# Kernel optimization log

Measured on AMD Instinct MI355X. Metric: run time of the kernel, lower is better.

Reference implementation:

```python
import jax, jax.numpy as jnp
import numpy as np

L, H, E, FF, MAXP, NKNOW = 4, 8, 512, 2048, 10, 1000
B, S = 4, 128
HD = E // H


def _layer_norm(x, g, b, eps=1e-5):
    m = x.mean(-1, keepdims=True)
    v = ((x - m) ** 2).mean(-1, keepdims=True)
    return (x - m) / jnp.sqrt(v + eps) * g + b


def setup_inputs() -> dict:
    key = jax.random.key(0)
    ks = jax.random.split(key, 16)
    x = jax.random.normal(ks[0], (B, S, E), jnp.float32)
    adj = jax.random.randint(ks[1], (B, S, S), 0, 2, jnp.int32)
    s_mask = jax.random.randint(ks[2], (B, S, S), 0, 2, jnp.int32)
    o_mask = jax.random.randint(ks[3], (B, S, S), 0, 2, jnp.int32)
    knowledge = jax.random.normal(ks[4], (NKNOW, E), jnp.float32)
    know_adj = jax.random.randint(ks[5], (B, S, S), 0, NKNOW, jnp.int64)
    pos_mask = jax.random.randint(ks[6], (S, S), 0, MAXP + 1, jnp.int32)
    # relative position embedding tables (padding_idx=0 -> row 0 zero)
    pe_k = jax.random.normal(ks[7], (MAXP + 1, HD), jnp.float32).at[0].set(0.0)
    pe_v = jax.random.normal(ks[8], (MAXP + 1, HD), jnp.float32).at[0].set(0.0)
    sc = 0.02
    # stacked per-layer parameters
    Wq = jax.random.normal(ks[9], (L, E, E), jnp.float32) * sc
    Wk = jax.random.normal(ks[10], (L, E, E), jnp.float32) * sc
    Wvs = jax.random.normal(ks[11], (L, E, E), jnp.float32) * sc
    Wvo = jax.random.normal(ks[12], (L, E, E), jnp.float32) * sc
    Wo = jax.random.normal(ks[13], (L, E, E), jnp.float32) * sc
    Wkn = jax.random.normal(ks[14], (L, E, E), jnp.float32) * sc
    kf = jax.random.split(ks[15], 4)
    w1 = jax.random.normal(kf[0], (L, FF, E), jnp.float32) * sc
    b1 = jnp.zeros((L, FF), jnp.float32)
    w2 = jax.random.normal(kf[1], (L, E, FF), jnp.float32) * sc
    b2 = jnp.zeros((L, E), jnp.float32)
    ln1_g = jnp.ones((L, E), jnp.float32)
    ln1_b = jnp.zeros((L, E), jnp.float32)
    ln2_g = jnp.ones((L, E), jnp.float32)
    ln2_b = jnp.zeros((L, E), jnp.float32)
    return dict(x=x, adj=adj, s_mask=s_mask, o_mask=o_mask, knowledge=knowledge,
                know_adj=know_adj, pos_mask=pos_mask, pe_k=pe_k, pe_v=pe_v,
                Wq=Wq, Wk=Wk, Wvs=Wvs, Wvo=Wvo, Wo=Wo, Wkn=Wkn,
                ln1_g=ln1_g, ln1_b=ln1_b, w1=w1, b1=b1, w2=w2, b2=b2,
                ln2_g=ln2_g, ln2_b=ln2_b)


def reference(x, adj, s_mask, o_mask, knowledge, know_adj, pos_mask, pe_k, pe_v,
              Wq, Wk, Wvs, Wvo, Wo, Wkn, ln1_g, ln1_b, w1, b1, w2, b2,
              ln2_g, ln2_b):
    bsz, slen, emb = x.shape
    hd = emb // H
    scaling = float(hd) ** (-0.5)
    # relative position embeddings, shared across batch/heads: [S,S,hd]
    pos = jnp.clip(pos_mask, 0, MAXP)
    rel_k = pe_k[pos]
    rel_v = pe_v[pos]
    adj_f = adj.astype(x.dtype)[:, None, :, :]          # [B,1,S,S]
    sm = s_mask.astype(x.dtype)[:, None, :, :, None]    # [B,1,S,S,1]
    om = o_mask.astype(x.dtype)[:, None, :, :, None]
    know_feat = knowledge[know_adj]                      # [B,S,S,E]

    def split_heads(t):  # [B,S,E] -> [B,H,S,hd]
        return t.reshape(bsz, slen, H, hd).transpose(0, 2, 1, 3)

    h = x
    for i in range(L):
        q = split_heads(h @ Wq[i].T)
        k = split_heads(h @ Wk[i].T)
        vs = split_heads(h @ Wvs[i].T)
        vo = split_heads(h @ Wvo[i].T)
        # knowledge projection -> [B,H,S,S,hd]
        know = (know_feat @ Wkn[i].T).reshape(bsz, slen, slen, H, hd).transpose(0, 3, 1, 2, 4)
        # multiplicative attention: q_i * (k_j + know_ij + rel_ij) summed over hd
        rel = (know + rel_k[None, None]) + k[:, :, None, :, :]
        scores = jnp.einsum('bhid,bhijd->bhij', q, rel) * scaling
        scores = scores - (1.0 - adj_f) * 1e30          # mask_logic
        attn = jax.nn.softmax(scores, axis=-1)           # [B,H,S,S]
        value = vs[:, :, None, :, :] * sm + vo[:, :, None, :, :] * om  # [B,H,S,S,hd]
        attn_sum = jnp.einsum('bhijd,bhij->bhid', value + rel_v[None, None], attn)
        out = attn_sum.transpose(0, 2, 1, 3).reshape(bsz, slen, emb) @ Wo[i].T
        h = _layer_norm(h + out, ln1_g[i], ln1_b[i])
        ff = jax.nn.relu(h @ w1[i].T + b1[i]) @ w2[i].T + b2[i]
        h = _layer_norm(h + ff, ln2_g[i], ln2_b[i])
    return h
```

## Files before the change

### kernel.cpp

```cpp
#include <hip/hip_runtime.h>

#define EE 512
#define SS 128
#define BB 4
#define NH 8
#define HD 64
#define FFD 2048
#define NL 4
#define LDQ 2048

typedef short bf16x8 __attribute__((ext_vector_type(8)));
typedef float f32x4 __attribute__((ext_vector_type(4)));

__device__ __forceinline__ ushort f2bf(float f) {
    uint u = __float_as_uint(f);
    return (ushort)((u + 0x7fffu + ((u >> 16) & 1u)) >> 16);
}
__device__ __forceinline__ float bflo(uint u) { return __uint_as_float(u << 16); }
__device__ __forceinline__ float bfhi(uint u) { return __uint_as_float(u & 0xffff0000u); }

__device__ __forceinline__ void gll16(const ushort* g, ushort* l) {
    __builtin_amdgcn_global_load_lds(
        (const __attribute__((address_space(1))) void*)g,
        (__attribute__((address_space(3))) void*)l, 16, 0, 0);
}

struct GemmJob {
    const ushort* A; const ushort* B;
    float* Cf; ushort* Cb;
    const float* bias; const float* resid;
    int M, N, K, flags, nbx, base;
};

__global__ __launch_bounds__(256) void gemm_bf16(GemmJob j0, GemmJob j1, int njobs)
{
    __shared__ ushort As[3][2048];
    __shared__ ushort Bs[3][4096];
    GemmJob j = (njobs > 1 && (int)blockIdx.x >= j1.base) ? j1 : j0;
    const int bid = (int)blockIdx.x - j.base;
    const int by = bid / j.nbx, bx = bid % j.nbx;
    const int rowBase = by * 32, colBase = bx * 64;
    const int t = threadIdx.x, lane = t & 63, wid = t >> 6;
    const int wc = wid;
    const int Kd = j.K, Md = j.M, Nd = j.N;

    const ushort* Bg = j.B + (size_t)(colBase + lane) * Kd;
    int gr = rowBase + (lane & 31); if (gr >= Md) gr = Md - 1;
    const ushort* Ag = j.A + (size_t)gr * Kd + (2 * wid + (lane >> 5)) * 8;

    f32x4 acc[2];
#pragma unroll
    for (int m = 0; m < 2; ++m)
#pragma unroll
        for (int r = 0; r < 4; ++r) acc[m][r] = 0.f;

    auto STAGE = [&](int bf, int tt) {
        const int k0 = tt << 6;
        gll16(Bg + k0 + (2 * wid) * 8,     &Bs[bf][(2 * wid) * 512]);
        gll16(Bg + k0 + (2 * wid + 1) * 8, &Bs[bf][(2 * wid + 1) * 512]);
        gll16(Ag + k0,                     &As[bf][(2 * wid) * 256]);
    };
    auto COMPUTE = [&](int bf) {
#pragma unroll
        for (int kc = 0; kc < 2; ++kc) {
            const int c16 = kc * 4 + (lane >> 4);
            bf16x8 af[2], bfg;
#pragma unroll
            for (int m = 0; m < 2; ++m) {
                const int row = m * 16 + (lane & 15);
                af[m] = *(const bf16x8*)&As[bf][c16 * 256 + row * 8];
            }
            {
                const int rowb = wc * 16 + (lane & 15);
                bfg = *(const bf16x8*)&Bs[bf][c16 * 512 + rowb * 8];
            }
#pragma unroll
            for (int m = 0; m < 2; ++m)
                acc[m] = __builtin_amdgcn_mfma_f32_16x16x32_bf16(af[m], bfg, acc[m], 0, 0, 0);
        }
    };

    const int nt = Kd >> 6;
    STAGE(0, 0);
    STAGE(1, 1);
    asm volatile("s_waitcnt vmcnt(3)" ::: "memory");
    __builtin_amdgcn_s_barrier();
    int bc = 0, bs = 2;
    for (int tt = 0; tt < nt; ++tt) {
        const bool more = (tt + 2) < nt;
        if (more) STAGE(bs, tt + 2);
        COMPUTE(bc);
        if (tt < nt - 1) {
            if (more) asm volatile("s_waitcnt vmcnt(3)" ::: "memory");
            else      asm volatile("s_waitcnt vmcnt(0)" ::: "memory");
            __builtin_amdgcn_s_barrier();
        }
        bc = bc == 2 ? 0 : bc + 1;
        bs = bs == 2 ? 0 : bs + 1;
    }

    const int cl = lane & 15, rh = lane >> 4;
#pragma unroll
    for (int m = 0; m < 2; ++m) {
        const int col = colBase + wc * 16 + cl;
        const int row0 = rowBase + m * 16 + rh * 4;
#pragma unroll
        for (int r = 0; r < 4; ++r) {
            const int rr = row0 + r;
            if (rr < Md) {
                float v = acc[m][r];
                if (j.flags & 1) v += j.bias[col];
                if (j.flags & 2) v = fmaxf(v, 0.f);
                if (j.resid) v += j.resid[(size_t)rr * Nd + col];
                if (j.Cf) j.Cf[(size_t)rr * Nd + col] = v;
                if (j.Cb) j.Cb[(size_t)rr * Nd + col] = f2bf(v);
            }
        }
    }
}

struct PrepArgs {
    const float *Wq, *Wk, *Wvs, *Wvo, *Wo, *Wkn, *w1, *w2, *know, *x;
    ushort *wqkvv, *wo, *wkn, *w1b, *w2b, *knowb, *hb;
    float *h;
};
#define P4_WQKVV 1048576
#define P4_B1 (P4_WQKVV + 262144)
#define P4_B2 (P4_B1 + 262144)
#define P4_B3 (P4_B2 + 1048576)
#define P4_B4 (P4_B3 + 1048576)
#define P4_B5 (P4_B4 + 128000)
#define P4_TOT (P4_B5 + 65536)

__global__ __launch_bounds__(256) void prep_kernel(PrepArgs p)
{
    const int i = blockIdx.x * 256 + threadIdx.x;
    if (i >= P4_TOT) return;
    const float4* src;
    ushort4* dst;
    if (i < P4_WQKVV) {
        const int l = i >> 18, r = i & 262143, q = r >> 16;
        const float* s = (q == 0 ? p.Wq : q == 1 ? p.Wk : q == 2 ? p.Wvs : p.Wvo);
        src = (const float4*)s + l * 65536 + (r & 65535);
        dst = (ushort4*)p.wqkvv + i;
    } else if (i < P4_B1) {
        const int k = i - P4_WQKVV;
        src = (const float4*)p.Wo + k; dst = (ushort4*)p.wo + k;
    } else if (i < P4_B2) {
        const int k = i - P4_B1;
        src = (const float4*)p.Wkn + k; dst = (ushort4*)p.wkn + k;
    } else if (i < P4_B3) {
        const int k = i - P4_B2;
        src = (const float4*)p.w1 + k; dst = (ushort4*)p.w1b + k;
    } else if (i < P4_B4) {
        const int k = i - P4_B3;
        src = (const float4*)p.w2 + k; dst = (ushort4*)p.w2b + k;
    } else if (i < P4_B5) {
        const int k = i - P4_B4;
        src = (const float4*)p.know + k; dst = (ushort4*)p.knowb + k;
    } else {
        const int k = i - P4_B5;
        src = (const float4*)p.x + k; dst = (ushort4*)p.hb + k;
        ((float4*)p.h)[k] = *src;
    }
    float4 v = *src;
    ushort4 o; o.x = f2bf(v.x); o.y = f2bf(v.y); o.z = f2bf(v.z); o.w = f2bf(v.w);
    *dst = o;
}

__global__ __launch_bounds__(256) void ln_kernel(
    const float* __restrict__ X, const float* __restrict__ g,
    const float* __restrict__ bt, float* __restrict__ Yf,
    ushort* __restrict__ Yb, int rows)
{
    const int w = threadIdx.x >> 6, lane = threadIdx.x & 63;
    const int row = blockIdx.x * 4 + w;
    if (row >= rows) return;
    const float* x = X + (size_t)row * EE;
    float4 v0 = ((const float4*)x)[lane];
    float4 v1 = ((const float4*)x)[lane + 64];
    float s  = v0.x + v0.y + v0.z + v0.w + v1.x + v1.y + v1.z + v1.w;
    float q2 = v0.x*v0.x + v0.y*v0.y + v0.z*v0.z + v0.w*v0.w
             + v1.x*v1.x + v1.y*v1.y + v1.z*v1.z + v1.w*v1.w;
#pragma unroll
    for (int o = 32; o; o >>= 1) { s += __shfl_xor(s, o); q2 += __shfl_xor(q2, o); }
    const float mean = s * (1.f / EE);
    const float var  = q2 * (1.f / EE) - mean * mean;
    const float rstd = rsqrtf(var + 1e-5f);
    float4 g0 = ((const float4*)g)[lane],  g1 = ((const float4*)g)[lane + 64];
    float4 b0 = ((const float4*)bt)[lane], b1 = ((const float4*)bt)[lane + 64];
    float4 o0, o1;
    o0.x = (v0.x - mean) * rstd * g0.x + b0.x;
    o0.y = (v0.y - mean) * rstd * g0.y + b0.y;
    o0.z = (v0.z - mean) * rstd * g0.z + b0.z;
    o0.w = (v0.w - mean) * rstd * g0.w + b0.w;
    o1.x = (v1.x - mean) * rstd * g1.x + b1.x;
    o1.y = (v1.y - mean) * rstd * g1.y + b1.y;
    o1.z = (v1.z - mean) * rstd * g1.z + b1.z;
    o1.w = (v1.w - mean) * rstd * g1.w + b1.w;
    float* y = Yf + (size_t)row * EE;
    ((float4*)y)[lane] = o0;
    ((float4*)y)[lane + 64] = o1;
    ushort* yb = Yb + (size_t)row * EE;
    ushort4 p0, p1;
    p0.x = f2bf(o0.x); p0.y = f2bf(o0.y); p0.z = f2bf(o0.z); p0.w = f2bf(o0.w);
    p1.x = f2bf(o1.x); p1.y = f2bf(o1.y); p1.z = f2bf(o1.z); p1.w = f2bf(o1.w);
    ((ushort4*)yb)[lane] = p0;
    ((ushort4*)yb)[lane + 64] = p1;
}

__global__ __launch_bounds__(256) void attn_kernel(
    const ushort* __restrict__ qkvv, const ushort* __restrict__ kproj,
    const int* __restrict__ know_adj, const int* __restrict__ pos_mask,
    const float* __restrict__ pe_k, const float* __restrict__ pe_v,
    const int* __restrict__ adj, const int* __restrict__ s_mask,
    const int* __restrict__ o_mask, ushort* __restrict__ asum)
{
    const int blk = blockIdx.x;
    const int b = blk >> 7, i = blk & 127;
    const int t = threadIdx.x;

    __shared__ float q_s[EE];
    __shared__ float sc[NH][SS];
    __shared__ float qpe[NH][11];
    __shared__ float ap[NH][11];
    __shared__ float ws_s[SS], wo_s[SS];
    __shared__ int   pos_s[SS], n_s[SS], adj_s[SS];

    if (t < 64) {
        uint4 v = *(const uint4*)(qkvv + (size_t)(b * SS + i) * LDQ + t * 8);
        float* qd = q_s + t * 8;
        qd[0] = bflo(v.x); qd[1] = bfhi(v.x); qd[2] = bflo(v.y); qd[3] = bfhi(v.y);
        qd[4] = bflo(v.z); qd[5] = bfhi(v.z); qd[6] = bflo(v.w); qd[7] = bfhi(v.w);
    } else if (t >= 128) {
        const int jj = t - 128;
        const size_t off = ((size_t)(b * SS + i)) * SS + jj;
        n_s[jj]   = know_adj[off];
        adj_s[jj] = adj[off];
        ws_s[jj]  = (float)s_mask[off];
        wo_s[jj]  = (float)o_mask[off];
        int p = pos_mask[i * SS + jj];
        pos_s[jj] = p > 10 ? 10 : (p < 0 ? 0 : p);
    }
    __syncthreads();

    if (t < NH * 11) {
        const int h = t / 11, p = t % 11;
        const float* pk = pe_k + p * HD;
        const float* qh = q_s + h * HD;
        float a = 0.f;
#pragma unroll
        for (int d = 0; d < HD; ++d) a += qh[d] * pk[d];
        qpe[h][p] = a;
        ap[h][p] = 0.f;
    }
    __syncthreads();

    {
        const int jj = t >> 1, s = t & 1;
        const uint4* kp4 = (const uint4*)(kproj + (size_t)n_s[jj] * LDQ + s * 256);
        const uint4* kr4 = (const uint4*)(qkvv + (size_t)(b * SS + jj) * LDQ + EE + s * 256);
        const float amask = adj_s[jj] ? 0.f : 1e30f;
        const int p = pos_s[jj];
#pragma unroll
        for (int h4 = 0; h4 < 4; ++h4) {
            const int h = s * 4 + h4;
            const float* qh = q_s + h * HD;
            float a = 0.f;
#pragma unroll
            for (int dv = 0; dv < 8; ++dv) {
                uint4 kv = kr4[h4 * 8 + dv];
                uint4 pv = kp4[h4 * 8 + dv];
                const float* q8 = qh + dv * 8;
                a += q8[0] * (bflo(kv.x) + bflo(pv.x));
                a += q8[1] * (bfhi(kv.x) + bfhi(pv.x));
                a += q8[2] * (bflo(kv.y) + bflo(pv.y));
                a += q8[3] * (bfhi(kv.y) + bfhi(pv.y));
                a += q8[4] * (bflo(kv.z) + bflo(pv.z));
                a += q8[5] * (bfhi(kv.z) + bfhi(pv.z));
                a += q8[6] * (bflo(kv.w) + bflo(pv.w));
                a += q8[7] * (bfhi(kv.w) + bfhi(pv.w));
            }
            sc[h][jj] = (a + qpe[h][p]) * 0.125f - amask;
        }
    }
    __syncthreads();

    {
        const int w = t >> 6, lane = t & 63;
#pragma unroll
        for (int hh = 0; hh < 2; ++hh) {
            const int h = w * 2 + hh;
            float v0 = sc[h][lane], v1 = sc[h][lane + 64];
            float m = fmaxf(v0, v1);
#pragma unroll
            for (int o = 32; o; o >>= 1) m = fmaxf(m, __shfl_xor(m, o));
            float e0 = __expf(v0 - m), e1 = __expf(v1 - m);
            float ssum = e0 + e1;
#pragma unroll
            for (int o = 32; o; o >>= 1) ssum += __shfl_xor(ssum, o);
            const float inv = 1.f / ssum;
            e0 *= inv; e1 *= inv;
            sc[h][lane] = e0; sc[h][lane + 64] = e1;
            atomicAdd(&ap[h][pos_s[lane]], e0);
            atomicAdd(&ap[h][pos_s[lane + 64]], e1);
        }
    }
    __syncthreads();

    {
        const int h = t >> 5, d0 = (t & 31) * 2;
        float a0 = 0.f, a1 = 0.f;
        const ushort* vbase = qkvv + (size_t)b * SS * LDQ + 1024 + h * HD + d0;
#pragma unroll 4
        for (int jj = 0; jj < SS; ++jj) {
            const float aw = sc[h][jj];
            const float wsj = ws_s[jj], woj = wo_s[jj];
            const ushort* r = vbase + (size_t)jj * LDQ;
            const uint vsp = *(const uint*)r;
            const uint vop = *(const uint*)(r + 512);
            a0 += aw * (wsj * bflo(vsp) + woj * bflo(vop));
            a1 += aw * (wsj * bfhi(vsp) + woj * bfhi(vop));
        }
#pragma unroll
        for (int p = 0; p < 11; ++p) {
            const float apv = ap[h][p];
            a0 += apv * pe_v[p * HD + d0];
            a1 += apv * pe_v[p * HD + d0 + 1];
        }
        const uint o = (uint)f2bf(a0) | ((uint)f2bf(a1) << 16);
        *(uint*)(asum + (size_t)(b * SS + i) * EE + h * HD + d0) = o;
    }
}

extern "C" void kernel_launch(void* const* d_in, const int* in_sizes, int n_in,
                              void* d_out, int out_size, void* d_ws, size_t ws_size,
                              hipStream_t stream)
{
    const float* x         = (const float*)d_in[0];
    const int*   adj       = (const int*)d_in[1];
    const int*   s_mask    = (const int*)d_in[2];
    const int*   o_mask    = (const int*)d_in[3];
    const float* knowledge = (const float*)d_in[4];
    const int*   know_adj  = (const int*)d_in[5];
    const int*   pos_mask  = (const int*)d_in[6];
    const float* pe_k      = (const float*)d_in[7];
    const float* pe_v      = (const float*)d_in[8];
    const float* Wq        = (const float*)d_in[9];
    const float* Wk        = (const float*)d_in[10];
    const float* Wvs       = (const float*)d_in[11];
    const float* Wvo       = (const float*)d_in[12];
    const float* Wo        = (const float*)d_in[13];
    const float* Wkn       = (const float*)d_in[14];
    const float* ln1_g     = (const float*)d_in[15];
    const float* ln1_b     = (const float*)d_in[16];
    const float* w1        = (const float*)d_in[17];
    const float* b1        = (const float*)d_in[18];
    const float* w2        = (const float*)d_in[19];
    const float* b2        = (const float*)d_in[20];
    const float* ln2_g     = (const float*)d_in[21];
    const float* ln2_b     = (const float*)d_in[22];

    const int NTOK = BB * SS;
    const size_t NTE = (size_t)NTOK * EE;

    float*  h      = (float*)d_ws;
    float*  xt     = h + NTE;
    ushort* hb     = (ushort*)(xt + NTE);
    ushort* qkvv   = hb + NTE;
    ushort* kprojb = qkvv + (size_t)NTOK * LDQ;
    ushort* asumb  = kprojb + (size_t)1024 * LDQ;
    ushort* ffnb   = asumb + NTE;
    ushort* wqkvv  = ffnb + (size_t)NTOK * FFD;
    ushort* wob    = wqkvv + (size_t)NL * 4 * EE * EE;
    ushort* wknb   = wob + (size_t)NL * EE * EE;
    ushort* w1b    = wknb + (size_t)NL * EE * EE;
    ushort* w2b    = w1b + (size_t)NL * FFD * EE;
    ushort* knowb  = w2b + (size_t)NL * EE * FFD;

    PrepArgs pa;
    pa.Wq = Wq; pa.Wk = Wk; pa.Wvs = Wvs; pa.Wvo = Wvo; pa.Wo = Wo; pa.Wkn = Wkn;
    pa.w1 = w1; pa.w2 = w2; pa.know = knowledge; pa.x = x;
    pa.wqkvv = wqkvv; pa.wo = wob; pa.wkn = wknb; pa.w1b = w1b; pa.w2b = w2b;
    pa.knowb = knowb; pa.hb = hb; pa.h = h;
    prep_kernel<<<dim3((P4_TOT + 255) / 256), dim3(256), 0, stream>>>(pa);

    const dim3 blk(256);
    for (int l = 0; l < NL; ++l) {
        GemmJob jq{};
        jq.A = hb; jq.B = wqkvv + (size_t)l * 4 * EE * EE;
        jq.Cb = qkvv; jq.M = NTOK; jq.N = 4 * EE; jq.K = EE;
        jq.nbx = 32; jq.base = 0;
        if (l == 0) {
            GemmJob jk{};
            jk.A = knowb; jk.B = wknb;
            jk.Cb = kprojb; jk.M = 1000; jk.N = NL * EE; jk.K = EE;
            jk.nbx = 32; jk.base = 512;
            gemm_bf16<<<dim3(512 + 1024), blk, 0, stream>>>(jq, jk, 2);
        } else {
            gemm_bf16<<<dim3(512), blk, 0, stream>>>(jq, jq, 1);
        }

        attn_kernel<<<dim3(NTOK), blk, 0, stream>>>(qkvv, kprojb + (size_t)l * EE,
                                                    know_adj, pos_mask,
                                                    pe_k, pe_v, adj, s_mask, o_mask, asumb);

        GemmJob jo{};
        jo.A = asumb; jo.B = wob + (size_t)l * EE * EE;
        jo.Cf = xt; jo.resid = h; jo.M = NTOK; jo.N = EE; jo.K = EE;
        jo.nbx = 8; jo.base = 0;
        gemm_bf16<<<dim3(128), blk, 0, stream>>>(jo, jo, 1);

        ln_kernel<<<dim3(128), blk, 0, stream>>>(xt, ln1_g + l * EE, ln1_b + l * EE,
                                                 h, hb, NTOK);

        GemmJob jf1{};
        jf1.A = hb; jf1.B = w1b + (size_t)l * FFD * EE;
        jf1.Cb = ffnb; jf1.bias = b1 + (size_t)l * FFD; jf1.flags = 3;
        jf1.M = NTOK; jf1.N = FFD; jf1.K = EE; jf1.nbx = 32; jf1.base = 0;
        gemm_bf16<<<dim3(512), blk, 0, stream>>>(jf1, jf1, 1);

        GemmJob jf2{};
        jf2.A = ffnb; jf2.B = w2b + (size_t)l * EE * FFD;
        jf2.Cf = xt; jf2.bias = b2 + (size_t)l * EE; jf2.resid = h; jf2.flags = 1;
        jf2.M = NTOK; jf2.N = EE; jf2.K = FFD; jf2.nbx = 8; jf2.base = 0;
        gemm_bf16<<<dim3(128), blk, 0, stream>>>(jf2, jf2, 1);

        float* lnout = (l == NL - 1) ? (float*)d_out : h;
        ln_kernel<<<dim3(128), blk, 0, stream>>>(xt, ln2_g + l * EE, ln2_b + l * EE,
                                                 lnout, hb, NTOK);
    }
}
```

Measured before the change: 578.2 us.

## Precompute attention score terms with MFMA GEMMs instead of per-pair dot products

Splits the score q·(k + know + rel_k) into three parts. The q·k part comes from a batched per-head MFMA GEMM. The q·know and q·pe_k parts come from one GEMM of every query against all 1000 knowledge projections plus 11 position-embedding rows, which are placed after the knowledge rows in the kproj buffer. The attention kernel then only gathers these precomputed scalars, which removes the per-(i,j) 64-wide gather dot products over bf16 rows. The value loop is also restructured to batch its loads. The trade-off is an extra kernel launch and large fp32 intermediates (qkk is 512×8192) written to and read back from global memory, which computes scores for all 1000 knowledge rows even though only gathered entries are used.

```diff
diff --git a/kernel.cpp b/kernel.cpp
--- a/kernel.cpp
+++ b/kernel.cpp
@@ -119,9 +119,79 @@
     }
 }
 
+__global__ __launch_bounds__(256) void score_gemm(
+    const ushort* __restrict__ qkvv, const ushort* __restrict__ kprojl,
+    float* __restrict__ qk, float* __restrict__ qkk)
+{
+    __shared__ ushort As[2048];
+    __shared__ ushort Bs[4096];
+    const int t = threadIdx.x, lane = t & 63, wid = t >> 6;
+    const int bid = blockIdx.x;
+    const ushort *Abase, *Bbase;
+    float* Cbase; int crs, rowBase, colBase;
+    if (bid < 256) {
+        const int q = bid >> 3, sub = bid & 7;
+        const int b = q >> 3, h = q & 7;
+        rowBase = (sub >> 1) * 32; colBase = (sub & 1) * 64;
+        Abase = qkvv + (size_t)(b * SS) * LDQ + h * HD;
+        Bbase = qkvv + (size_t)(b * SS) * LDQ + 512 + h * HD;
+        Cbase = qk + (size_t)b * 131072 + h * 128;
+        crs = 1024;
+    } else {
+        const int idx = bid - 256;
+        const int h = idx >> 8, sub = idx & 255;
+        rowBase = (sub >> 4) * 32; colBase = (sub & 15) * 64;
+        Abase = qkvv + h * HD;
+        Bbase = kprojl + h * HD;
+        Cbase = qkk + (size_t)h * 1024;
+        crs = 8192;
+    }
+    {
+        const ushort* Bg = Bbase + (size_t)(colBase + lane) * LDQ;
+        const ushort* Ag = Abase + (size_t)(rowBase + (lane & 31)) * LDQ
+                           + (2 * wid + (lane >> 5)) * 8;
+        gll16(Bg + (2 * wid) * 8,     &Bs[(2 * wid) * 512]);
+        gll16(Bg + (2 * wid + 1) * 8, &Bs[(2 * wid + 1) * 512]);
+        gll16(Ag,                     &As[(2 * wid) * 256]);
+        asm volatile("s_waitcnt vmcnt(0)" ::: "memory");
+        __builtin_amdgcn_s_barrier();
+    }
+    f32x4 acc[2];
+#pragma unroll
+    for (int m = 0; m < 2; ++m)
+#pragma unroll
+        for (int r = 0; r < 4; ++r) acc[m][r] = 0.f;
+#pragma unroll
+    for (int kc = 0; kc < 2; ++kc) {
+        const int c16 = kc * 4 + (lane >> 4);
+        bf16x8 af[2], bfg;
+#pragma unroll
+        for (int m = 0; m < 2; ++m) {
+            const int row = m * 16 + (lane & 15);
+            af[m] = *(const bf16x8*)&As[c16 * 256 + row * 8];
+        }
+        {
+            const int rowb = wid * 16 + (lane & 15);
+            bfg = *(const bf16x8*)&Bs[c16 * 512 + rowb * 8];
+        }
+#pragma unroll
+        for (int m = 0; m < 2; ++m)
+            acc[m] = __builtin_amdgcn_mfma_f32_16x16x32_bf16(af[m], bfg, acc[m], 0, 0, 0);
+    }
+    const int cl = lane & 15, rh = lane >> 4;
+#pragma unroll
+    for (int m = 0; m < 2; ++m) {
+        const int col = colBase + wid * 16 + cl;
+        const int row0 = rowBase + m * 16 + rh * 4;
+#pragma unroll
+        for (int r = 0; r < 4; ++r)
+            Cbase[(size_t)(row0 + r) * crs + col] = acc[m][r];
+    }
+}
+
 struct PrepArgs {
-    const float *Wq, *Wk, *Wvs, *Wvo, *Wo, *Wkn, *w1, *w2, *know, *x;
-    ushort *wqkvv, *wo, *wkn, *w1b, *w2b, *knowb, *hb;
+    const float *Wq, *Wk, *Wvs, *Wvo, *Wo, *Wkn, *w1, *w2, *know, *x, *pek;
+    ushort *wqkvv, *wo, *wkn, *w1b, *w2b, *knowb, *hb, *kpe;
     float *h;
 };
 #define P4_WQKVV 1048576
@@ -130,9 +200,10 @@
 #define P4_B3 (P4_B2 + 1048576)
 #define P4_B4 (P4_B3 + 1048576)
 #define P4_B5 (P4_B4 + 128000)
-#define P4_TOT (P4_B5 + 65536)
-
-__global__ __launch_bounds__(256) void prep_kernel(PrepArgs p)
+#define P4_B6 (P4_B5 + 65536)
+#define P4_TOT (P4_B6 + 5632)
+
+__global__ __launch_bounds__(256) void prep_kernel(PrepArgs pa)
 {
     const int i = blockIdx.x * 256 + threadIdx.x;
     if (i >= P4_TOT) return;
@@ -140,28 +211,34 @@
     ushort4* dst;
     if (i < P4_WQKVV) {
         const int l = i >> 18, r = i & 262143, q = r >> 16;
-        const float* s = (q == 0 ? p.Wq : q == 1 ? p.Wk : q == 2 ? p.Wvs : p.Wvo);
+        const float* s = (q == 0 ? pa.Wq : q == 1 ? pa.Wk : q == 2 ? pa.Wvs : pa.Wvo);
         src = (const float4*)s + l * 65536 + (r & 65535);
-        dst = (ushort4*)p.wqkvv + i;
+        dst = (ushort4*)pa.wqkvv + i;
     } else if (i < P4_B1) {
         const int k = i - P4_WQKVV;
-        src = (const float4*)p.Wo + k; dst = (ushort4*)p.wo + k;
+        src = (const float4*)pa.Wo + k; dst = (ushort4*)pa.wo + k;
     } else if (i < P4_B2) {
         const int k = i - P4_B1;
-        src = (const float4*)p.Wkn + k; dst = (ushort4*)p.wkn + k;
+        src = (const float4*)pa.Wkn + k; dst = (ushort4*)pa.wkn + k;
     } else if (i < P4_B3) {
         const int k = i - P4_B2;
-        src = (const float4*)p.w1 + k; dst = (ushort4*)p.w1b + k;
+        src = (const float4*)pa.w1 + k; dst = (ushort4*)pa.w1b + k;
     } else if (i < P4_B4) {
         const int k = i - P4_B3;
-        src = (const float4*)p.w2 + k; dst = (ushort4*)p.w2b + k;
+        src = (const float4*)pa.w2 + k; dst = (ushort4*)pa.w2b + k;
     } else if (i < P4_B5) {
         const int k = i - P4_B4;
-        src = (const float4*)p.know + k; dst = (ushort4*)p.knowb + k;
+        src = (const float4*)pa.know + k; dst = (ushort4*)pa.knowb + k;
+    } else if (i < P4_B6) {
+        const int k = i - P4_B5;
+        src = (const float4*)pa.x + k; dst = (ushort4*)pa.hb + k;
+        ((float4*)pa.h)[k] = *src;
     } else {
-        const int k = i - P4_B5;
-        src = (const float4*)p.x + k; dst = (ushort4*)p.hb + k;
-        ((float4*)p.h)[k] = *src;
+        const int k = i - P4_B6;
+        const int c4 = k * 4;
+        const int p = c4 >> 11, col = c4 & 2047, d = col & 63;
+        src = (const float4*)(pa.pek + p * 64 + d);
+        dst = (ushort4*)(pa.kpe + (size_t)(1000 + p) * 2048 + col);
     }
     float4 v = *src;
     ushort4 o; o.x = f2bf(v.x); o.y = f2bf(v.y); o.z = f2bf(v.z); o.w = f2bf(v.w);
@@ -210,9 +287,10 @@
 }
 
 __global__ __launch_bounds__(256) void attn_kernel(
-    const ushort* __restrict__ qkvv, const ushort* __restrict__ kproj,
+    const ushort* __restrict__ qkvv, const float* __restrict__ qk,
+    const float* __restrict__ qkk,
     const int* __restrict__ know_adj, const int* __restrict__ pos_mask,
-    const float* __restrict__ pe_k, const float* __restrict__ pe_v,
+    const float* __restrict__ pe_v,
     const int* __restrict__ adj, const int* __restrict__ s_mask,
     const int* __restrict__ o_mask, ushort* __restrict__ asum)
 {
@@ -220,68 +298,39 @@
     const int b = blk >> 7, i = blk & 127;
     const int t = threadIdx.x;
 
-    __shared__ float q_s[EE];
     __shared__ float sc[NH][SS];
-    __shared__ float qpe[NH][11];
     __shared__ float ap[NH][11];
-    __shared__ float ws_s[SS], wo_s[SS];
-    __shared__ int   pos_s[SS], n_s[SS], adj_s[SS];
-
-    if (t < 64) {
-        uint4 v = *(const uint4*)(qkvv + (size_t)(b * SS + i) * LDQ + t * 8);
-        float* qd = q_s + t * 8;
-        qd[0] = bflo(v.x); qd[1] = bfhi(v.x); qd[2] = bflo(v.y); qd[3] = bfhi(v.y);
-        qd[4] = bflo(v.z); qd[5] = bfhi(v.z); qd[6] = bflo(v.w); qd[7] = bfhi(v.w);
-    } else if (t >= 128) {
-        const int jj = t - 128;
+    __shared__ float ws_s[SS], wo_s[SS], amask_s[SS];
+    __shared__ int   pos_s[SS], n_s[SS];
+
+    const float* qkrow  = qk + (size_t)b * 131072 + (size_t)i * 1024;
+    const float* qkkrow = qkk + (size_t)(b * SS + i) * 8192;
+
+    if (t < 128) {
+        const int jj = t;
         const size_t off = ((size_t)(b * SS + i)) * SS + jj;
-        n_s[jj]   = know_adj[off];
-        adj_s[jj] = adj[off];
-        ws_s[jj]  = (float)s_mask[off];
-        wo_s[jj]  = (float)o_mask[off];
+        n_s[jj]     = know_adj[off];
+        amask_s[jj] = adj[off] ? 0.f : 1e30f;
+        ws_s[jj]    = (float)s_mask[off];
+        wo_s[jj]    = (float)o_mask[off];
         int p = pos_mask[i * SS + jj];
         pos_s[jj] = p > 10 ? 10 : (p < 0 ? 0 : p);
+        if (t < 88) ap[t / 11][t % 11] = 0.f;
+    } else {
+        const int tt = t - 128;
+        ((float4*)&sc[0][0])[tt]       = ((const float4*)qkrow)[tt];
+        ((float4*)&sc[0][0])[tt + 128] = ((const float4*)qkrow)[tt + 128];
     }
     __syncthreads();
 
-    if (t < NH * 11) {
-        const int h = t / 11, p = t % 11;
-        const float* pk = pe_k + p * HD;
-        const float* qh = q_s + h * HD;
-        float a = 0.f;
-#pragma unroll
-        for (int d = 0; d < HD; ++d) a += qh[d] * pk[d];
-        qpe[h][p] = a;
-        ap[h][p] = 0.f;
-    }
-    __syncthreads();
-
     {
-        const int jj = t >> 1, s = t & 1;
-        const uint4* kp4 = (const uint4*)(kproj + (size_t)n_s[jj] * LDQ + s * 256);
-        const uint4* kr4 = (const uint4*)(qkvv + (size_t)(b * SS + jj) * LDQ + EE + s * 256);
-        const float amask = adj_s[jj] ? 0.f : 1e30f;
-        const int p = pos_s[jj];
-#pragma unroll
-        for (int h4 = 0; h4 < 4; ++h4) {
-            const int h = s * 4 + h4;
-            const float* qh = q_s + h * HD;
-            float a = 0.f;
-#pragma unroll
-            for (int dv = 0; dv < 8; ++dv) {
-                uint4 kv = kr4[h4 * 8 + dv];
-                uint4 pv = kp4[h4 * 8 + dv];
-                const float* q8 = qh + dv * 8;
-                a += q8[0] * (bflo(kv.x) + bflo(pv.x));
-                a += q8[1] * (bfhi(kv.x) + bfhi(pv.x));
-                a += q8[2] * (bflo(kv.y) + bflo(pv.y));
-                a += q8[3] * (bfhi(kv.y) + bfhi(pv.y));
-                a += q8[4] * (bflo(kv.z) + bflo(pv.z));
-                a += q8[5] * (bfhi(kv.z) + bfhi(pv.z));
-                a += q8[6] * (bflo(kv.w) + bflo(pv.w));
-                a += q8[7] * (bfhi(kv.w) + bfhi(pv.w));
-            }
-            sc[h][jj] = (a + qpe[h][p]) * 0.125f - amask;
+        const int h = t >> 5, j0 = (t & 31) * 4;
+        const float* qh = qkkrow + h * 1024;
+#pragma unroll
+        for (int u = 0; u < 4; ++u) {
+            const int jj = j0 + u;
+            const float v = sc[h][jj] + qh[n_s[jj]] + qh[1000 + pos_s[jj]];
+            sc[h][jj] = v * 0.125f - amask_s[jj];
         }
     }
     __syncthreads();
@@ -312,15 +361,22 @@
         const int h = t >> 5, d0 = (t & 31) * 2;
         float a0 = 0.f, a1 = 0.f;
         const ushort* vbase = qkvv + (size_t)b * SS * LDQ + 1024 + h * HD + d0;
-#pragma unroll 4
-        for (int jj = 0; jj < SS; ++jj) {
-            const float aw = sc[h][jj];
-            const float wsj = ws_s[jj], woj = wo_s[jj];
-            const ushort* r = vbase + (size_t)jj * LDQ;
-            const uint vsp = *(const uint*)r;
-            const uint vop = *(const uint*)(r + 512);
-            a0 += aw * (wsj * bflo(vsp) + woj * bflo(vop));
-            a1 += aw * (wsj * bfhi(vsp) + woj * bfhi(vop));
+        for (int j0 = 0; j0 < SS; j0 += 8) {
+            uint vsp[8], vop[8];
+#pragma unroll
+            for (int u = 0; u < 8; ++u) {
+                const ushort* r = vbase + (size_t)(j0 + u) * LDQ;
+                vsp[u] = *(const uint*)r;
+                vop[u] = *(const uint*)(r + 512);
+            }
+#pragma unroll
+            for (int u = 0; u < 8; ++u) {
+                const int jj = j0 + u;
+                const float aw = sc[h][jj];
+                const float wsj = ws_s[jj], woj = wo_s[jj];
+                a0 += aw * (wsj * bflo(vsp[u]) + woj * bflo(vop[u]));
+                a1 += aw * (wsj * bfhi(vsp[u]) + woj * bfhi(vop[u]));
+            }
         }
 #pragma unroll
         for (int p = 0; p < 11; ++p) {
@@ -366,7 +422,9 @@
 
     float*  h      = (float*)d_ws;
     float*  xt     = h + NTE;
-    ushort* hb     = (ushort*)(xt + NTE);
+    float*  qk     = xt + NTE;
+    float*  qkk    = qk + (size_t)NTOK * 1024;
+    ushort* hb     = (ushort*)(qkk + (size_t)NTOK * 8192);
     ushort* qkvv   = hb + NTE;
     ushort* kprojb = qkvv + (size_t)NTOK * LDQ;
     ushort* asumb  = kprojb + (size_t)1024 * LDQ;
@@ -380,9 +438,9 @@
 
     PrepArgs pa;
     pa.Wq = Wq; pa.Wk = Wk; pa.Wvs = Wvs; pa.Wvo = Wvo; pa.Wo = Wo; pa.Wkn = Wkn;
-    pa.w1 = w1; pa.w2 = w2; pa.know = knowledge; pa.x = x;
+    pa.w1 = w1; pa.w2 = w2; pa.know = knowledge; pa.x = x; pa.pek = pe_k;
     pa.wqkvv = wqkvv; pa.wo = wob; pa.wkn = wknb; pa.w1b = w1b; pa.w2b = w2b;
-    pa.knowb = knowb; pa.hb = hb; pa.h = h;
+    pa.knowb = knowb; pa.hb = hb; pa.h = h; pa.kpe = kprojb;
     prep_kernel<<<dim3((P4_TOT + 255) / 256), dim3(256), 0, stream>>>(pa);
 
     const dim3 blk(256);
@@ -401,9 +459,12 @@
             gemm_bf16<<<dim3(512), blk, 0, stream>>>(jq, jq, 1);
         }
 
-        attn_kernel<<<dim3(NTOK), blk, 0, stream>>>(qkvv, kprojb + (size_t)l * EE,
-                                                    know_adj, pos_mask,
-                                                    pe_k, pe_v, adj, s_mask, o_mask, asumb);
+        score_gemm<<<dim3(2304), blk, 0, stream>>>(qkvv, kprojb + (size_t)l * EE,
+                                                   qk, qkk);
+
+        attn_kernel<<<dim3(NTOK), blk, 0, stream>>>(qkvv, qk, qkk,
+                                                    know_adj, pos_mask, pe_v,
+                                                    adj, s_mask, o_mask, asumb);
 
         GemmJob jo{};
         jo.A = asumb; jo.B = wob + (size_t)l * EE * EE;
```

New measurement: 525.9 us. 9.0% less time.
